# Kernel tuning notes

Hardware: AMD Instinct MI355X
Metric: run time of the kernel (lower is better)

Reference implementation:

```python
import jax, jax.numpy as jnp
import numpy as np

N = 50000          # nodes (cells)
G = 1000           # input genes
E = 800000         # edges
HIDDEN = 128
HEADS = 8
C_HID = HIDDEN // HEADS   # 16 per-head channels
LATENT = 16
NEG_SLOPE = 0.2


def _gat_layer(x, src, dst, W, a_src, a_dst, b, heads, out_ch, concat):
    """PyG GATConv (shared lin for src/dst, add_self_loops=False, eval mode)."""
    n = x.shape[0]
    h = (x @ W).reshape(n, heads, out_ch)                 # [N,H,C]
    al_s = jnp.einsum('nhc,hc->nh', h, a_src)             # [N,H]
    al_d = jnp.einsum('nhc,hc->nh', h, a_dst)             # [N,H]
    logits = jax.nn.leaky_relu(al_s[src] + al_d[dst], NEG_SLOPE)  # [E,H]
    # segment softmax over destination neighborhoods
    m = jax.ops.segment_max(logits, dst, num_segments=n)  # [N,H]
    m = jnp.where(jnp.isfinite(m), m, 0.0)                # empty segments -> 0
    e = jnp.exp(logits - m[dst])                          # [E,H]
    denom = jax.ops.segment_sum(e, dst, num_segments=n)   # [N,H]
    alpha = e / (denom[dst] + 1e-16)                      # [E,H]
    msg = h[src] * alpha[:, :, None]                      # [E,H,C]
    out = jax.ops.segment_sum(msg, dst, num_segments=n)   # [N,H,C]
    out = out.reshape(n, heads * out_ch) if concat else out.mean(axis=1)
    return out + b


def setup_inputs() -> dict:
    key = jax.random.key(0)
    ks = jax.random.split(key, 16)
    x = jax.random.normal(ks[0], (N, G), dtype=jnp.float32)
    edge_index = jax.random.randint(ks[1], (2, E), 0, N, dtype=jnp.int64)

    def glorot(k, shape):
        fan_in, fan_out = shape[0], shape[-1]
        s = jnp.sqrt(6.0 / (fan_in + fan_out)).astype(jnp.float32)
        return jax.random.uniform(k, shape, jnp.float32, -s, s)

    # layer 0: G -> 8 heads x 16 (concat -> 128)
    W0 = glorot(ks[2], (G, HEADS * C_HID))
    as0 = glorot(ks[3], (HEADS, C_HID))
    ad0 = glorot(ks[4], (HEADS, C_HID))
    b0 = jnp.zeros((HEADS * C_HID,), jnp.float32)
    # layer 1: 128 -> 8 heads x 16 (concat -> 128)
    W1 = glorot(ks[5], (HIDDEN, HEADS * C_HID))
    as1 = glorot(ks[6], (HEADS, C_HID))
    ad1 = glorot(ks[7], (HEADS, C_HID))
    b1 = jnp.zeros((HEADS * C_HID,), jnp.float32)
    # layer 2: 128 -> 1 head x 16 (concat=False -> 16)
    W2 = glorot(ks[8], (HIDDEN, LATENT))
    as2 = glorot(ks[9], (1, LATENT))
    ad2 = glorot(ks[10], (1, LATENT))
    b2 = jnp.zeros((LATENT,), jnp.float32)

    return {"x": x, "edge_index": edge_index,
            "W0": W0, "as0": as0, "ad0": ad0, "b0": b0,
            "W1": W1, "as1": as1, "ad1": ad1, "b1": b1,
            "W2": W2, "as2": as2, "ad2": ad2, "b2": b2}


def reference(x, edge_index, W0, as0, ad0, b0, W1, as1, ad1, b1, W2, as2, ad2, b2):
    src, dst = edge_index[0], edge_index[1]
    h = _gat_layer(x, src, dst, W0, as0, ad0, b0, HEADS, C_HID, concat=True)
    h = jax.nn.elu(h)
    h = _gat_layer(h, src, dst, W1, as1, ad1, b1, HEADS, C_HID, concat=True)
    h = jax.nn.elu(h)
    z = _gat_layer(h, src, dst, W2, as2, ad2, b2, 1, LATENT, concat=False)
    return z
```

## Files before the change

### kernel.cpp

```cpp
#include <hip/hip_runtime.h>
#include <hip/hip_bf16.h>
#include <math.h>

#define GENES 1000

typedef __attribute__((ext_vector_type(8))) _Float16 half8;
typedef __attribute__((ext_vector_type(4))) float f32x4;
typedef __attribute__((ext_vector_type(4))) unsigned int uint4v;
typedef __attribute__((ext_vector_type(2))) unsigned int uint2v;

__device__ inline float f16lo(unsigned int v) {
  return (float)__builtin_bit_cast(_Float16, (unsigned short)(v & 0xffffu));
}
__device__ inline float f16hi(unsigned int v) {
  return (float)__builtin_bit_cast(_Float16, (unsigned short)(v >> 16));
}
__device__ inline unsigned int pk(float a, float b) {
  return __builtin_bit_cast(unsigned int, __builtin_amdgcn_cvt_pkrtz(a, b));
}

__device__ inline void gload16(const void* g, void* l) {
  __builtin_amdgcn_global_load_lds(
      (const __attribute__((address_space(1))) unsigned int*)g,
      (__attribute__((address_space(3))) unsigned int*)l, 16, 0, 0);
}

__device__ __forceinline__ void waitvm(int n) {
  __builtin_amdgcn_sched_barrier(0);
  if (n <= 0)      asm volatile("s_waitcnt vmcnt(0)" ::: "memory");
  else             asm volatile("s_waitcnt vmcnt(2)" ::: "memory");
  __builtin_amdgcn_sched_barrier(0);
}


__global__ void k_scan1(int* __restrict__ deg, int* __restrict__ ptr,
                        int* __restrict__ bsum, int n) {
  __shared__ int ws[4];
  int t = threadIdx.x, b = blockIdx.x;
  int i = b * 256 + t;
  int lane = t & 63, w = t >> 6;
  int x = 0;
  if (i < n) { x = deg[i]; deg[i] = 0; }
  #pragma unroll
  for (int d = 1; d < 64; d <<= 1) {
    int y = __shfl_up(x, d);
    if (lane >= d) x += y;
  }
  if (lane == 63) ws[w] = x;
  __syncthreads();
  if (t == 0) {
    int s = 0;
    #pragma unroll
    for (int k = 0; k < 4; ++k) { s += ws[k]; ws[k] = s; }
  }
  __syncthreads();
  int incl = x + (w ? ws[w - 1] : 0);
  if (i < n) ptr[i + 1] = incl;
  if (t == 255) bsum[b] = incl;
  if (i == 0) ptr[0] = 0;
}

__global__ void k_scan2(int* __restrict__ bsum, int nb) {
  __shared__ int ws[4];
  int t = threadIdx.x;
  int lane = t & 63, w = t >> 6;
  int v = (t < nb) ? bsum[t] : 0;
  int x = v;
  #pragma unroll
  for (int d = 1; d < 64; d <<= 1) {
    int y = __shfl_up(x, d);
    if (lane >= d) x += y;
  }
  if (lane == 63) ws[w] = x;
  __syncthreads();
  if (t == 0) {
    int s = 0;
    #pragma unroll
    for (int k = 0; k < 4; ++k) { s += ws[k]; ws[k] = s; }
  }
  __syncthreads();
  int incl = x + (w ? ws[w - 1] : 0);
  if (t < nb) bsum[t] = incl - v;
}

__global__ void k_scan3(int* __restrict__ ptr, const int* __restrict__ bsum, int n) {
  int i = blockIdx.x * 256 + threadIdx.x;
  if (i < n) ptr[i + 1] += bsum[blockIdx.x];
}


__global__ void k_wpackdeg(const float* __restrict__ W0, const float* __restrict__ W1,
                           const float* __restrict__ W2, unsigned short* __restrict__ P,
                           int K0, const int* __restrict__ ei, int* __restrict__ deg,
                           int E) {
  int t = blockIdx.x * blockDim.x + threadIdx.x;
  if (t < 163840) {
    const float* W; int K, N, e;
    if (t < 131072)      { W = W0; K = K0;  N = 128; e = t; }
    else if (t < 147456) { W = W1; K = 128; N = 128; e = t - 131072; }
    else                 { W = W2; K = 128; N = 16;  e = t - 147456; }
    int s = e >> 12, rem = e & 4095;
    int q = rem >> 10, col = (rem >> 3) & 127, j = rem & 7;
    int k = s * 32 + q * 8 + j;
    float v = (k < K && col < N) ? W[(long)k * N + col] : 0.f;
    _Float16 h = (_Float16)v;
    P[t] = __builtin_bit_cast(unsigned short, h);
  }
  if (t < E) atomicAdd(&deg[ei[E + t]], 1);
}


__global__ __launch_bounds__(512) void k_mgemm14(
    const float* __restrict__ A, const unsigned short* __restrict__ Pb,
    unsigned short* __restrict__ outp, float* __restrict__ als,
    float* __restrict__ ald, const float* __restrict__ avs,
    const float* __restrict__ avd, int M, int K,
    const int* __restrict__ ei, const int* __restrict__ ptr,
    int* __restrict__ cur, int* __restrict__ srcs, int E) {
  __shared__ __align__(16) char lds[49152];

  int t = threadIdx.x, lane = t & 63, wv = t >> 6;
  int r15 = lane & 15, q = lane >> 4;
  int wr = wv >> 1, wc = wv & 1;
  long row0 = (long)blockIdx.x * 64;

  int srow = t >> 3, sseg = t & 7;
  int gseg = sseg ^ (srow & 7);
  long arow = row0 + srow; if (arow >= M) arow = M - 1;
  const char* gA = (const char*)(A + arow * (long)K) + gseg * 16;
  const char* gB = (const char*)Pb + t * 16;

  f32x4 acc[4];
  #pragma unroll
  for (int nt = 0; nt < 4; ++nt) acc[nt] = (f32x4){0.f, 0.f, 0.f, 0.f};

  auto issue = [&](int s) {
    char* Ab = lds + (s % 3) * 8192;
    char* Bb = lds + 24576 + (s % 3) * 8192;
    gload16(gA + (size_t)s * 128, Ab + t * 16);
    gload16(gB + (size_t)s * 8192, Bb + t * 16);
  };
  auto compute = [&](int s) {
    const char* Ab = lds + (s % 3) * 8192;
    const char* Bb = lds + 24576 + (s % 3) * 8192;
    int row = wr * 16 + r15;
    int sw = row & 7;
    uint4v alo = *(const uint4v*)(Ab + row * 128 + ((2 * q) ^ sw) * 16);
    uint4v ahi = *(const uint4v*)(Ab + row * 128 + ((2 * q + 1) ^ sw) * 16);
    float4 lo = __builtin_bit_cast(float4, alo);
    float4 hi = __builtin_bit_cast(float4, ahi);
    uint4v au;
    au[0] = pk(lo.x, lo.y); au[1] = pk(lo.z, lo.w);
    au[2] = pk(hi.x, hi.y); au[3] = pk(hi.z, hi.w);
    half8 af = __builtin_bit_cast(half8, au);
    #pragma unroll
    for (int nt = 0; nt < 4; ++nt) {
      half8 bf = *(const half8*)(Bb + q * 2048 + (wc * 64 + nt * 16 + r15) * 16);
      acc[nt] = __builtin_amdgcn_mfma_f32_16x16x32_f16(af, bf, acc[nt], 0, 0, 0);
    }
  };

  issue(0); issue(1);

  {
    int e0 = blockIdx.x * 1024 + t;
    if (e0 < E) {
      int d = ei[E + e0];
      int pos = ptr[d] + atomicAdd(&cur[d], 1);
      srcs[pos] = ei[e0];
    }
    int e1 = e0 + 512;
    if (e1 < E) {
      int d = ei[E + e1];
      int pos = ptr[d] + atomicAdd(&cur[d], 1);
      srcs[pos] = ei[e1];
    }
  }

  #pragma unroll
  for (int s = 0; s < 32; ++s) {
    waitvm(s < 31 ? 2 : 0);
    __builtin_amdgcn_s_barrier();
    compute(s);
    if (s + 2 < 32) issue(s + 2);
  }

  long rbase = row0 + wr * 16 + q * 4;
  #pragma unroll
  for (int i = 0; i < 4; ++i) {
    long r = rbase + i;
    if (r < M) {
      #pragma unroll
      for (int nt = 0; nt < 4; ++nt) {
        int col = wc * 64 + nt * 16 + r15;
        _Float16 hv = (_Float16)acc[nt][i];
        outp[r * 128 + col] = __builtin_bit_cast(unsigned short, hv);
      }
    }
  }
  #pragma unroll
  for (int nt = 0; nt < 4; ++nt) {
    int head = wc * 4 + nt;
    float cs = avs[head * 16 + r15];
    float cd = avd[head * 16 + r15];
    #pragma unroll
    for (int i = 0; i < 4; ++i) {
      float s1 = acc[nt][i] * cs;
      float s2 = acc[nt][i] * cd;
      #pragma unroll
      for (int d = 1; d < 16; d <<= 1) {
        s1 += __shfl_xor(s1, d);
        s2 += __shfl_xor(s2, d);
      }
      if (r15 == 0) {
        long r = rbase + i;
        if (r < M) { als[r * 8 + head] = s1; ald[r * 8 + head] = s2; }
      }
    }
  }
}


template<int HH, bool AF16, bool OF16>
__global__ __launch_bounds__(512) void k_mgemm7(
    const void* __restrict__ Ap, const unsigned short* __restrict__ Pb,
    void* __restrict__ outp, float* __restrict__ als, float* __restrict__ ald,
    const float* __restrict__ avs, const float* __restrict__ avd,
    int M, int K, int nst, int ldc) {
  __shared__ __align__(16) char lds[24576];
  char* bA0 = lds;
  char* bA1 = lds + 4096;
  char* bB0 = lds + 8192;
  char* bB1 = lds + 16384;

  int t = threadIdx.x, lane = t & 63;
  int r15 = lane & 15, q = lane >> 4;
  int wv = t >> 6;
  int wr = wv >> 1, wc = wv & 1;
  long row0 = (long)blockIdx.x * 64;

  int srow = t >> 3, sseg = t & 7;
  long arow = row0 + srow; if (arow >= M) arow = M - 1;
  const float* pa32 = (const float*)Ap + arow * (long)K;
  const unsigned short* pa16 = (const unsigned short*)Ap + arow * (long)K;

  f32x4 acc[4];
  #pragma unroll
  for (int nt = 0; nt < 4; ++nt) acc[nt] = (f32x4){0.f, 0.f, 0.f, 0.f};

  uint4v rA0, rA1, rB0, rB1;
  uint2v sA0, sA1;

  auto loadA = [&](int s, uint4v& r32, uint2v& r16) {
    int k0 = s * 32 + sseg * 4;
    if constexpr (AF16) {
      r16 = (k0 < K) ? *(const uint2v*)(pa16 + k0) : (uint2v){0u, 0u};
    } else {
      r32 = (k0 < K) ? *(const uint4v*)(pa32 + k0) : (uint4v){0u, 0u, 0u, 0u};
    }
  };
  auto writeA = [&](char* buf, uint4v r32, uint2v r16) {
    char* p = buf + ((sseg >> 1) * 1024 + srow * 16 + (sseg & 1) * 8);
    if constexpr (AF16) {
      *(uint2v*)p = r16;
    } else {
      float4 f = __builtin_bit_cast(float4, r32);
      uint2v h;
      h[0] = pk(f.x, f.y);
      h[1] = pk(f.z, f.w);
      *(uint2v*)p = h;
    }
  };
  auto loadB = [&](int s, uint4v& r) {
    r = *(const uint4v*)(Pb + (size_t)s * 4096 + t * 8);
  };
  auto writeB = [&](char* buf, uint4v r) {
    *(uint4v*)(buf + t * 16) = r;
  };
  auto compute = [&](const char* bA, const char* bB) {
    half8 af = *(const half8*)(bA + q * 1024 + (wr * 16 + r15) * 16);
    #pragma unroll
    for (int nt = 0; nt < 4; ++nt) {
      half8 bf = *(const half8*)(bB + q * 2048 + (wc * 64 + nt * 16 + r15) * 16);
      acc[nt] = __builtin_amdgcn_mfma_f32_16x16x32_f16(af, bf, acc[nt], 0, 0, 0);
    }
  };

  loadA(0, rA0, sA0); loadB(0, rB0);
  if (nst > 1) { loadA(1, rA1, sA1); loadB(1, rB1); }
  writeA(bA0, rA0, sA0); writeB(bB0, rB0);
  __syncthreads();

  for (int s = 0; s < nst; s += 2) {
    if (s + 2 < nst) { loadA(s + 2, rA0, sA0); loadB(s + 2, rB0); }
    compute(bA0, bB0);
    if (s + 1 < nst) { writeA(bA1, rA1, sA1); writeB(bB1, rB1); }
    __syncthreads();
    if (s + 1 < nst) {
      if (s + 3 < nst) { loadA(s + 3, rA1, sA1); loadB(s + 3, rB1); }
      compute(bA1, bB1);
      if (s + 2 < nst) { writeA(bA0, rA0, sA0); writeB(bB0, rB0); }
      __syncthreads();
    }
  }

  long rbase = row0 + wr * 16 + q * 4;
  if constexpr (OF16) {
    unsigned short* o16 = (unsigned short*)outp;
    #pragma unroll
    for (int i = 0; i < 4; ++i) {
      long r = rbase + i;
      if (r < M) {
        #pragma unroll
        for (int nt = 0; nt < 4; ++nt) {
          int col = wc * 64 + nt * 16 + r15;
          _Float16 hv = (_Float16)acc[nt][i];
          o16[r * ldc + col] = __builtin_bit_cast(unsigned short, hv);
        }
      }
    }
  } else {
    float* o32 = (float*)outp;
    #pragma unroll
    for (int i = 0; i < 4; ++i) {
      long r = rbase + i;
      if (r < M) {
        #pragma unroll
        for (int nt = 0; nt < 4; ++nt) {
          int col = wc * 64 + nt * 16 + r15;
          if (col < ldc) o32[r * ldc + col] = acc[nt][i];
        }
      }
    }
  }
  #pragma unroll
  for (int nt = 0; nt < 4; ++nt) {
    int head = wc * 4 + nt;
    if (head < HH) {
      float cs = avs[head * 16 + r15];
      float cd = avd[head * 16 + r15];
      #pragma unroll
      for (int i = 0; i < 4; ++i) {
        float s1 = acc[nt][i] * cs;
        float s2 = acc[nt][i] * cd;
        #pragma unroll
        for (int d = 1; d < 16; d <<= 1) {
          s1 += __shfl_xor(s1, d);
          s2 += __shfl_xor(s2, d);
        }
        if (r15 == 0) {
          long r = rbase + i;
          if (r < M) { als[r * HH + head] = s1; ald[r * HH + head] = s2; }
        }
      }
    }
  }
}


__global__ void k_agg128h(const unsigned short* __restrict__ h,
                          const float* __restrict__ als, const float* __restrict__ ald,
                          const int* __restrict__ ptr, const int* __restrict__ srcs,
                          const float* __restrict__ bias,
                          unsigned short* __restrict__ out, int n) {
  int wid = (int)(((long)blockIdx.x * blockDim.x + threadIdx.x) >> 6);
  if (wid >= n) return;
  int lane = threadIdx.x & 63;
  int half = lane >> 5, l5 = lane & 31;
  int c0 = 4 * l5;
  int hB = l5 >> 2;
  int p0 = ptr[wid], deg = ptr[wid + 1] - p0;
  float aldB = ald[wid * 8 + hB];
  float a0 = 0.f, a1 = 0.f, a2 = 0.f, a3 = 0.f, dsum = 0.f;
  int j = half;
  for (; j + 6 < deg; j += 8) {
    int s0 = srcs[p0 + j],     s1 = srcs[p0 + j + 2];
    int s2 = srcs[p0 + j + 4], s3 = srcs[p0 + j + 6];
    float l0 = als[s0 * 8 + hB] + aldB;
    float l1 = als[s1 * 8 + hB] + aldB;
    float l2 = als[s2 * 8 + hB] + aldB;
    float l3 = als[s3 * 8 + hB] + aldB;
    uint2v h0 = *(const uint2v*)(h + (long)s0 * 128 + c0);
    uint2v h1 = *(const uint2v*)(h + (long)s1 * 128 + c0);
    uint2v h2 = *(const uint2v*)(h + (long)s2 * 128 + c0);
    uint2v h3 = *(const uint2v*)(h + (long)s3 * 128 + c0);
    l0 = l0 > 0.f ? l0 : 0.2f * l0;
    l1 = l1 > 0.f ? l1 : 0.2f * l1;
    l2 = l2 > 0.f ? l2 : 0.2f * l2;
    l3 = l3 > 0.f ? l3 : 0.2f * l3;
    float e0 = __expf(l0), e1 = __expf(l1), e2 = __expf(l2), e3 = __expf(l3);
    dsum += e0 + e1 + e2 + e3;
    a0 += e0 * f16lo(h0[0]) + e1 * f16lo(h1[0]) + e2 * f16lo(h2[0]) + e3 * f16lo(h3[0]);
    a1 += e0 * f16hi(h0[0]) + e1 * f16hi(h1[0]) + e2 * f16hi(h2[0]) + e3 * f16hi(h3[0]);
    a2 += e0 * f16lo(h0[1]) + e1 * f16lo(h1[1]) + e2 * f16lo(h2[1]) + e3 * f16lo(h3[1]);
    a3 += e0 * f16hi(h0[1]) + e1 * f16hi(h1[1]) + e2 * f16hi(h2[1]) + e3 * f16hi(h3[1]);
  }
  for (; j < deg; j += 2) {
    int s = srcs[p0 + j];
    float l = als[s * 8 + hB] + aldB;
    l = l > 0.f ? l : 0.2f * l;
    float e = __expf(l);
    uint2v hv = *(const uint2v*)(h + (long)s * 128 + c0);
    dsum += e;
    a0 += e * f16lo(hv[0]);
    a1 += e * f16hi(hv[0]);
    a2 += e * f16lo(hv[1]);
    a3 += e * f16hi(hv[1]);
  }
  a0 += __shfl_xor(a0, 32);
  a1 += __shfl_xor(a1, 32);
  a2 += __shfl_xor(a2, 32);
  a3 += __shfl_xor(a3, 32);
  dsum += __shfl_xor(dsum, 32);
  if (half == 0) {
    float inv = 1.f / (dsum + 1e-16f);
    float o0 = a0 * inv + bias[c0];
    float o1 = a1 * inv + bias[c0 + 1];
    float o2 = a2 * inv + bias[c0 + 2];
    float o3 = a3 * inv + bias[c0 + 3];
    o0 = o0 > 0.f ? o0 : (__expf(o0) - 1.f);
    o1 = o1 > 0.f ? o1 : (__expf(o1) - 1.f);
    o2 = o2 > 0.f ? o2 : (__expf(o2) - 1.f);
    o3 = o3 > 0.f ? o3 : (__expf(o3) - 1.f);
    uint2v po;
    po[0] = __builtin_bit_cast(unsigned int, __builtin_amdgcn_cvt_pkrtz(o0, o1));
    po[1] = __builtin_bit_cast(unsigned int, __builtin_amdgcn_cvt_pkrtz(o2, o3));
    *(uint2v*)(out + (long)wid * 128 + c0) = po;
  }
}


__global__ void k_agg16(const float* __restrict__ h, const float* __restrict__ als,
                        const float* __restrict__ ald, const int* __restrict__ ptr,
                        const int* __restrict__ srcs, const float* __restrict__ bias,
                        float* __restrict__ out, int n, int lda) {
  int wid = (int)(((long)blockIdx.x * blockDim.x + threadIdx.x) >> 6);
  if (wid >= n) return;
  int lane = threadIdx.x & 63;
  int p0 = ptr[wid], deg = ptr[wid + 1] - p0;
  float aldv = ald[wid];
  int g = lane >> 4, c = lane & 15;
  float acc = 0.f, dsum = 0.f;
  int j = g;
  for (; j + 12 < deg; j += 16) {
    int s0 = srcs[p0 + j],     s1 = srcs[p0 + j + 4];
    int s2 = srcs[p0 + j + 8], s3 = srcs[p0 + j + 12];
    float l0 = als[s0] + aldv, l1 = als[s1] + aldv;
    float l2 = als[s2] + aldv, l3 = als[s3] + aldv;
    float h0 = h[(long)s0 * lda + c], h1 = h[(long)s1 * lda + c];
    float h2 = h[(long)s2 * lda + c], h3 = h[(long)s3 * lda + c];
    l0 = l0 > 0.f ? l0 : 0.2f * l0;
    l1 = l1 > 0.f ? l1 : 0.2f * l1;
    l2 = l2 > 0.f ? l2 : 0.2f * l2;
    l3 = l3 > 0.f ? l3 : 0.2f * l3;
    float e0 = __expf(l0), e1 = __expf(l1), e2 = __expf(l2), e3 = __expf(l3);
    dsum += e0 + e1 + e2 + e3;
    acc += e0 * h0 + e1 * h1 + e2 * h2 + e3 * h3;
  }
  for (; j < deg; j += 4) {
    int s = srcs[p0 + j];
    float l = als[s] + aldv;
    l = l > 0.f ? l : 0.2f * l;
    float e = __expf(l);
    dsum += e;
    acc += e * h[(long)s * lda + c];
  }
  #pragma unroll
  for (int d = 16; d < 64; d <<= 1) {
    acc += __shfl_xor(acc, d);
    dsum += __shfl_xor(dsum, d);
  }
  if (lane < 16)
    out[(long)wid * 16 + lane] = acc / (dsum + 1e-16f) + bias[lane];
}


extern "C" void kernel_launch(void* const* d_in, const int* in_sizes, int n_in,
                              void* d_out, int out_size, void* d_ws, size_t ws_size,
                              hipStream_t stream) {
  const float* x  = (const float*)d_in[0];
  const int*   ei = (const int*)d_in[1];
  const float* W0 = (const float*)d_in[2];
  const float* as0= (const float*)d_in[3];
  const float* ad0= (const float*)d_in[4];
  const float* b0 = (const float*)d_in[5];
  const float* W1 = (const float*)d_in[6];
  const float* as1= (const float*)d_in[7];
  const float* ad1= (const float*)d_in[8];
  const float* b1 = (const float*)d_in[9];
  const float* W2 = (const float*)d_in[10];
  const float* as2= (const float*)d_in[11];
  const float* ad2= (const float*)d_in[12];
  const float* b2 = (const float*)d_in[13];
  float* out = (float*)d_out;

  int E = in_sizes[1] / 2;
  int n = in_sizes[0] / GENES;

  char* ws = (char*)d_ws;
  size_t off = 0;
  auto alloc = [&](size_t bytes) {
    void* p = ws + off;
    off = (off + bytes + 255) & ~(size_t)255;
    return p;
  };
  int* ptr   = (int*)alloc((size_t)(n + 1) * sizeof(int));
  int* cur   = (int*)alloc((size_t)n * sizeof(int));
  int* bsum  = (int*)alloc(512 * sizeof(int));
  int* srcs  = (int*)alloc((size_t)E * sizeof(int));
  unsigned short* Ah = (unsigned short*)alloc((size_t)n * 128 * sizeof(unsigned short));
  unsigned short* Bh = (unsigned short*)alloc((size_t)n * 128 * sizeof(unsigned short));
  float* A2  = (float*)alloc((size_t)n * 16 * sizeof(float));
  float* als = (float*)alloc((size_t)n * 8 * sizeof(float));
  float* ald = (float*)alloc((size_t)n * 8 * sizeof(float));
  unsigned short* P = (unsigned short*)alloc((size_t)163840 * sizeof(unsigned short));
  unsigned short* P0 = P;
  unsigned short* P1 = P + 131072;
  unsigned short* P2 = P + 147456;

  int eb = (E + 255) / 256;
  int nb = (n + 255) / 256;
  hipMemsetAsync(cur, 0, (size_t)n * sizeof(int), stream);
  k_wpackdeg<<<eb, 256, 0, stream>>>(W0, W1, W2, P, GENES, ei, cur, E);
  k_scan1<<<nb, 256, 0, stream>>>(cur, ptr, bsum, n);
  k_scan2<<<1, 256, 0, stream>>>(bsum, nb);
  k_scan3<<<nb, 256, 0, stream>>>(ptr, bsum, n);

  int mgb  = (n + 63) / 64;
  int aggb = (int)(((long)n * 64 + 255) / 256);

  k_mgemm14<<<mgb, 512, 0, stream>>>(x, P0, Ah, als, ald, as0, ad0, n, GENES,
                                     ei, ptr, cur, srcs, E);
  k_agg128h<<<aggb, 256, 0, stream>>>(Ah, als, ald, ptr, srcs, b0, Bh, n);

  k_mgemm7<8, true, true><<<mgb, 512, 0, stream>>>(
      Bh, P1, Ah, als, ald, as1, ad1, n, 128, 4, 128);
  k_agg128h<<<aggb, 256, 0, stream>>>(Ah, als, ald, ptr, srcs, b1, Bh, n);

  k_mgemm7<1, true, false><<<mgb, 512, 0, stream>>>(
      Bh, P2, A2, als, ald, as2, ad2, n, 128, 4, 16);
  k_agg16<<<aggb, 256, 0, stream>>>(A2, als, ald, ptr, srcs, b2, out, n, 16);
}
```

Before: 262.9 us.

## Fuse neighbor aggregation with following layer's projection GEMM via LDS tile

Replaces the separate aggregation kernel and the next layer's GEMM with one kernel. Each block aggregates 64 destination rows into an fp16 tile in LDS, applying softmax weighting, bias and ELU, then multiplies that tile by the packed weights straight from global memory. This removes the round trip of the intermediate hidden activations through global memory and one launch per layer. In exchange, the attention logits now need separate buffers per layer. The aggregation also now runs 8 nodes per wave serially inside a 512-thread block, which may lower the parallelism available to hide gather latency.

```diff
diff --git a/kernel.cpp b/kernel.cpp
--- a/kernel.cpp
+++ b/kernel.cpp
@@ -221,86 +221,107 @@
 }
 
 
-template<int HH, bool AF16, bool OF16>
-__global__ __launch_bounds__(512) void k_mgemm7(
-    const void* __restrict__ Ap, const unsigned short* __restrict__ Pb,
-    void* __restrict__ outp, float* __restrict__ als, float* __restrict__ ald,
+template<int HH, bool OF16>
+__global__ __launch_bounds__(512) void k_fagg(
+    const unsigned short* __restrict__ hsrc,
+    const float* __restrict__ als_i, const float* __restrict__ ald_i,
+    const int* __restrict__ ptr, const int* __restrict__ srcs,
+    const float* __restrict__ bias, const unsigned short* __restrict__ Pb,
+    void* __restrict__ outp, float* __restrict__ als_o, float* __restrict__ ald_o,
     const float* __restrict__ avs, const float* __restrict__ avd,
-    int M, int K, int nst, int ldc) {
-  __shared__ __align__(16) char lds[24576];
-  char* bA0 = lds;
-  char* bA1 = lds + 4096;
-  char* bB0 = lds + 8192;
-  char* bB1 = lds + 16384;
-
-  int t = threadIdx.x, lane = t & 63;
+    int M, int ldc) {
+  __shared__ __align__(16) unsigned short At[4 * 4 * 64 * 8];
+
+  int t = threadIdx.x, lane = t & 63, wv = t >> 6;
+  int half = lane >> 5, l5 = lane & 31;
+  long row0 = (long)blockIdx.x * 64;
+
+  int c0 = 4 * l5;
+  int hB = l5 >> 2;
+  int sA = c0 >> 5, qA = (c0 >> 3) & 3, jA = c0 & 7;
+  #pragma unroll 1
+  for (int i = 0; i < 8; ++i) {
+    int rowL = wv * 8 + i;
+    long node = row0 + rowL;
+    char* dst = (char*)At + ((sA * 4 + qA) * 64 + rowL) * 16 + (jA ? 8 : 0);
+    if (node < M) {
+      int p0 = ptr[node], deg = ptr[node + 1] - p0;
+      float aldB = ald_i[node * 8 + hB];
+      float a0 = 0.f, a1 = 0.f, a2 = 0.f, a3 = 0.f, dsum = 0.f;
+      int j = half;
+      for (; j + 6 < deg; j += 8) {
+        int s0 = srcs[p0 + j],     s1 = srcs[p0 + j + 2];
+        int s2 = srcs[p0 + j + 4], s3 = srcs[p0 + j + 6];
+        float l0 = als_i[s0 * 8 + hB] + aldB;
+        float l1 = als_i[s1 * 8 + hB] + aldB;
+        float l2 = als_i[s2 * 8 + hB] + aldB;
+        float l3 = als_i[s3 * 8 + hB] + aldB;
+        uint2v h0 = *(const uint2v*)(hsrc + (long)s0 * 128 + c0);
+        uint2v h1 = *(const uint2v*)(hsrc + (long)s1 * 128 + c0);
+        uint2v h2 = *(const uint2v*)(hsrc + (long)s2 * 128 + c0);
+        uint2v h3 = *(const uint2v*)(hsrc + (long)s3 * 128 + c0);
+        l0 = l0 > 0.f ? l0 : 0.2f * l0;
+        l1 = l1 > 0.f ? l1 : 0.2f * l1;
+        l2 = l2 > 0.f ? l2 : 0.2f * l2;
+        l3 = l3 > 0.f ? l3 : 0.2f * l3;
+        float e0 = __expf(l0), e1 = __expf(l1), e2 = __expf(l2), e3 = __expf(l3);
+        dsum += e0 + e1 + e2 + e3;
+        a0 += e0 * f16lo(h0[0]) + e1 * f16lo(h1[0]) + e2 * f16lo(h2[0]) + e3 * f16lo(h3[0]);
+        a1 += e0 * f16hi(h0[0]) + e1 * f16hi(h1[0]) + e2 * f16hi(h2[0]) + e3 * f16hi(h3[0]);
+        a2 += e0 * f16lo(h0[1]) + e1 * f16lo(h1[1]) + e2 * f16lo(h2[1]) + e3 * f16lo(h3[1]);
+        a3 += e0 * f16hi(h0[1]) + e1 * f16hi(h1[1]) + e2 * f16hi(h2[1]) + e3 * f16hi(h3[1]);
+      }
+      for (; j < deg; j += 2) {
+        int s = srcs[p0 + j];
+        float l = als_i[s * 8 + hB] + aldB;
+        l = l > 0.f ? l : 0.2f * l;
+        float e = __expf(l);
+        uint2v hv = *(const uint2v*)(hsrc + (long)s * 128 + c0);
+        dsum += e;
+        a0 += e * f16lo(hv[0]);
+        a1 += e * f16hi(hv[0]);
+        a2 += e * f16lo(hv[1]);
+        a3 += e * f16hi(hv[1]);
+      }
+      a0 += __shfl_xor(a0, 32);
+      a1 += __shfl_xor(a1, 32);
+      a2 += __shfl_xor(a2, 32);
+      a3 += __shfl_xor(a3, 32);
+      dsum += __shfl_xor(dsum, 32);
+      if (half == 0) {
+        float inv = 1.f / (dsum + 1e-16f);
+        float o0 = a0 * inv + bias[c0];
+        float o1 = a1 * inv + bias[c0 + 1];
+        float o2 = a2 * inv + bias[c0 + 2];
+        float o3 = a3 * inv + bias[c0 + 3];
+        o0 = o0 > 0.f ? o0 : (__expf(o0) - 1.f);
+        o1 = o1 > 0.f ? o1 : (__expf(o1) - 1.f);
+        o2 = o2 > 0.f ? o2 : (__expf(o2) - 1.f);
+        o3 = o3 > 0.f ? o3 : (__expf(o3) - 1.f);
+        uint2v pv;
+        pv[0] = pk(o0, o1);
+        pv[1] = pk(o2, o3);
+        *(uint2v*)dst = pv;
+      }
+    } else if (half == 0) {
+      *(uint2v*)dst = (uint2v){0u, 0u};
+    }
+  }
+  __syncthreads();
+
   int r15 = lane & 15, q = lane >> 4;
-  int wv = t >> 6;
   int wr = wv >> 1, wc = wv & 1;
-  long row0 = (long)blockIdx.x * 64;
-
-  int srow = t >> 3, sseg = t & 7;
-  long arow = row0 + srow; if (arow >= M) arow = M - 1;
-  const float* pa32 = (const float*)Ap + arow * (long)K;
-  const unsigned short* pa16 = (const unsigned short*)Ap + arow * (long)K;
-
   f32x4 acc[4];
   #pragma unroll
   for (int nt = 0; nt < 4; ++nt) acc[nt] = (f32x4){0.f, 0.f, 0.f, 0.f};
-
-  uint4v rA0, rA1, rB0, rB1;
-  uint2v sA0, sA1;
-
-  auto loadA = [&](int s, uint4v& r32, uint2v& r16) {
-    int k0 = s * 32 + sseg * 4;
-    if constexpr (AF16) {
-      r16 = (k0 < K) ? *(const uint2v*)(pa16 + k0) : (uint2v){0u, 0u};
-    } else {
-      r32 = (k0 < K) ? *(const uint4v*)(pa32 + k0) : (uint4v){0u, 0u, 0u, 0u};
-    }
-  };
-  auto writeA = [&](char* buf, uint4v r32, uint2v r16) {
-    char* p = buf + ((sseg >> 1) * 1024 + srow * 16 + (sseg & 1) * 8);
-    if constexpr (AF16) {
-      *(uint2v*)p = r16;
-    } else {
-      float4 f = __builtin_bit_cast(float4, r32);
-      uint2v h;
-      h[0] = pk(f.x, f.y);
-      h[1] = pk(f.z, f.w);
-      *(uint2v*)p = h;
-    }
-  };
-  auto loadB = [&](int s, uint4v& r) {
-    r = *(const uint4v*)(Pb + (size_t)s * 4096 + t * 8);
-  };
-  auto writeB = [&](char* buf, uint4v r) {
-    *(uint4v*)(buf + t * 16) = r;
-  };
-  auto compute = [&](const char* bA, const char* bB) {
-    half8 af = *(const half8*)(bA + q * 1024 + (wr * 16 + r15) * 16);
+  #pragma unroll
+  for (int s = 0; s < 4; ++s) {
+    half8 af = *(const half8*)((const char*)At + ((s * 4 + q) * 64 + wr * 16 + r15) * 16);
     #pragma unroll
     for (int nt = 0; nt < 4; ++nt) {
-      half8 bf = *(const half8*)(bB + q * 2048 + (wc * 64 + nt * 16 + r15) * 16);
+      int col = wc * 64 + nt * 16 + r15;
+      half8 bf = *(const half8*)((const char*)Pb + (size_t)s * 8192 + q * 2048 + col * 16);
       acc[nt] = __builtin_amdgcn_mfma_f32_16x16x32_f16(af, bf, acc[nt], 0, 0, 0);
-    }
-  };
-
-  loadA(0, rA0, sA0); loadB(0, rB0);
-  if (nst > 1) { loadA(1, rA1, sA1); loadB(1, rB1); }
-  writeA(bA0, rA0, sA0); writeB(bB0, rB0);
-  __syncthreads();
-
-  for (int s = 0; s < nst; s += 2) {
-    if (s + 2 < nst) { loadA(s + 2, rA0, sA0); loadB(s + 2, rB0); }
-    compute(bA0, bB0);
-    if (s + 1 < nst) { writeA(bA1, rA1, sA1); writeB(bB1, rB1); }
-    __syncthreads();
-    if (s + 1 < nst) {
-      if (s + 3 < nst) { loadA(s + 3, rA1, sA1); loadB(s + 3, rB1); }
-      compute(bA1, bB1);
-      if (s + 2 < nst) { writeA(bA0, rA0, sA0); writeB(bB0, rB0); }
-      __syncthreads();
     }
   }
 
@@ -350,82 +371,10 @@
         }
         if (r15 == 0) {
           long r = rbase + i;
-          if (r < M) { als[r * HH + head] = s1; ald[r * HH + head] = s2; }
+          if (r < M) { als_o[r * HH + head] = s1; ald_o[r * HH + head] = s2; }
         }
       }
     }
-  }
-}
-
-
-__global__ void k_agg128h(const unsigned short* __restrict__ h,
-                          const float* __restrict__ als, const float* __restrict__ ald,
-                          const int* __restrict__ ptr, const int* __restrict__ srcs,
-                          const float* __restrict__ bias,
-                          unsigned short* __restrict__ out, int n) {
-  int wid = (int)(((long)blockIdx.x * blockDim.x + threadIdx.x) >> 6);
-  if (wid >= n) return;
-  int lane = threadIdx.x & 63;
-  int half = lane >> 5, l5 = lane & 31;
-  int c0 = 4 * l5;
-  int hB = l5 >> 2;
-  int p0 = ptr[wid], deg = ptr[wid + 1] - p0;
-  float aldB = ald[wid * 8 + hB];
-  float a0 = 0.f, a1 = 0.f, a2 = 0.f, a3 = 0.f, dsum = 0.f;
-  int j = half;
-  for (; j + 6 < deg; j += 8) {
-    int s0 = srcs[p0 + j],     s1 = srcs[p0 + j + 2];
-    int s2 = srcs[p0 + j + 4], s3 = srcs[p0 + j + 6];
-    float l0 = als[s0 * 8 + hB] + aldB;
-    float l1 = als[s1 * 8 + hB] + aldB;
-    float l2 = als[s2 * 8 + hB] + aldB;
-    float l3 = als[s3 * 8 + hB] + aldB;
-    uint2v h0 = *(const uint2v*)(h + (long)s0 * 128 + c0);
-    uint2v h1 = *(const uint2v*)(h + (long)s1 * 128 + c0);
-    uint2v h2 = *(const uint2v*)(h + (long)s2 * 128 + c0);
-    uint2v h3 = *(const uint2v*)(h + (long)s3 * 128 + c0);
-    l0 = l0 > 0.f ? l0 : 0.2f * l0;
-    l1 = l1 > 0.f ? l1 : 0.2f * l1;
-    l2 = l2 > 0.f ? l2 : 0.2f * l2;
-    l3 = l3 > 0.f ? l3 : 0.2f * l3;
-    float e0 = __expf(l0), e1 = __expf(l1), e2 = __expf(l2), e3 = __expf(l3);
-    dsum += e0 + e1 + e2 + e3;
-    a0 += e0 * f16lo(h0[0]) + e1 * f16lo(h1[0]) + e2 * f16lo(h2[0]) + e3 * f16lo(h3[0]);
-    a1 += e0 * f16hi(h0[0]) + e1 * f16hi(h1[0]) + e2 * f16hi(h2[0]) + e3 * f16hi(h3[0]);
-    a2 += e0 * f16lo(h0[1]) + e1 * f16lo(h1[1]) + e2 * f16lo(h2[1]) + e3 * f16lo(h3[1]);
-    a3 += e0 * f16hi(h0[1]) + e1 * f16hi(h1[1]) + e2 * f16hi(h2[1]) + e3 * f16hi(h3[1]);
-  }
-  for (; j < deg; j += 2) {
-    int s = srcs[p0 + j];
-    float l = als[s * 8 + hB] + aldB;
-    l = l > 0.f ? l : 0.2f * l;
-    float e = __expf(l);
-    uint2v hv = *(const uint2v*)(h + (long)s * 128 + c0);
-    dsum += e;
-    a0 += e * f16lo(hv[0]);
-    a1 += e * f16hi(hv[0]);
-    a2 += e * f16lo(hv[1]);
-    a3 += e * f16hi(hv[1]);
-  }
-  a0 += __shfl_xor(a0, 32);
-  a1 += __shfl_xor(a1, 32);
-  a2 += __shfl_xor(a2, 32);
-  a3 += __shfl_xor(a3, 32);
-  dsum += __shfl_xor(dsum, 32);
-  if (half == 0) {
-    float inv = 1.f / (dsum + 1e-16f);
-    float o0 = a0 * inv + bias[c0];
-    float o1 = a1 * inv + bias[c0 + 1];
-    float o2 = a2 * inv + bias[c0 + 2];
-    float o3 = a3 * inv + bias[c0 + 3];
-    o0 = o0 > 0.f ? o0 : (__expf(o0) - 1.f);
-    o1 = o1 > 0.f ? o1 : (__expf(o1) - 1.f);
-    o2 = o2 > 0.f ? o2 : (__expf(o2) - 1.f);
-    o3 = o3 > 0.f ? o3 : (__expf(o3) - 1.f);
-    uint2v po;
-    po[0] = __builtin_bit_cast(unsigned int, __builtin_amdgcn_cvt_pkrtz(o0, o1));
-    po[1] = __builtin_bit_cast(unsigned int, __builtin_amdgcn_cvt_pkrtz(o2, o3));
-    *(uint2v*)(out + (long)wid * 128 + c0) = po;
   }
 }
 
@@ -510,9 +459,13 @@
   int* srcs  = (int*)alloc((size_t)E * sizeof(int));
   unsigned short* Ah = (unsigned short*)alloc((size_t)n * 128 * sizeof(unsigned short));
   unsigned short* Bh = (unsigned short*)alloc((size_t)n * 128 * sizeof(unsigned short));
-  float* A2  = (float*)alloc((size_t)n * 16 * sizeof(float));
-  float* als = (float*)alloc((size_t)n * 8 * sizeof(float));
-  float* ald = (float*)alloc((size_t)n * 8 * sizeof(float));
+  float* A2   = (float*)alloc((size_t)n * 16 * sizeof(float));
+  float* als0 = (float*)alloc((size_t)n * 8 * sizeof(float));
+  float* ald0 = (float*)alloc((size_t)n * 8 * sizeof(float));
+  float* als1 = (float*)alloc((size_t)n * 8 * sizeof(float));
+  float* ald1 = (float*)alloc((size_t)n * 8 * sizeof(float));
+  float* als2 = (float*)alloc((size_t)n * sizeof(float));
+  float* ald2 = (float*)alloc((size_t)n * sizeof(float));
   unsigned short* P = (unsigned short*)alloc((size_t)163840 * sizeof(unsigned short));
   unsigned short* P0 = P;
   unsigned short* P1 = P + 131072;
@@ -529,15 +482,14 @@
   int mgb  = (n + 63) / 64;
   int aggb = (int)(((long)n * 64 + 255) / 256);
 
-  k_mgemm14<<<mgb, 512, 0, stream>>>(x, P0, Ah, als, ald, as0, ad0, n, GENES,
+  k_mgemm14<<<mgb, 512, 0, stream>>>(x, P0, Ah, als0, ald0, as0, ad0, n, GENES,
                                      ei, ptr, cur, srcs, E);
-  k_agg128h<<<aggb, 256, 0, stream>>>(Ah, als, ald, ptr, srcs, b0, Bh, n);
-
-  k_mgemm7<8, true, true><<<mgb, 512, 0, stream>>>(
-      Bh, P1, Ah, als, ald, as1, ad1, n, 128, 4, 128);
-  k_agg128h<<<aggb, 256, 0, stream>>>(Ah, als, ald, ptr, srcs, b1, Bh, n);
-
-  k_mgemm7<1, true, false><<<mgb, 512, 0, stream>>>(
-      Bh, P2, A2, als, ald, as2, ad2, n, 128, 4, 16);
-  k_agg16<<<aggb, 256, 0, stream>>>(A2, als, ald, ptr, srcs, b2, out, n, 16);
-}
+
+  k_fagg<8, true><<<mgb, 512, 0, stream>>>(
+      Ah, als0, ald0, ptr, srcs, b0, P1, Bh, als1, ald1, as1, ad1, n, 128);
+
+  k_fagg<1, false><<<mgb, 512, 0, stream>>>(
+      Bh, als1, ald1, ptr, srcs, b1, P2, A2, als2, ald2, as2, ad2, n, 16);
+
+  k_agg16<<<aggb, 256, 0, stream>>>(A2, als2, ald2, ptr, srcs, b2, out, n, 16);
+}
```

Result: faster. 255.5 us (-2.8%).
